# Optimization experiments

Measured on AMD Instinct MI355X. Metric: run time of the kernel, lower is better.

The kernel has to match this reference:

```python
import jax, jax.numpy as jnp
import numpy as np


def conv1x1(x, w, b):
    # x: [B,C,H,W], w: [O,C], b: [O]
    return jnp.einsum('bchw,oc->bohw', x, w) + b[None, :, None, None]


def conv3x3(x, w, b):
    # x: [B,C,H,W], w: [O,C,3,3]
    y = jax.lax.conv_general_dilated(
        x, w, window_strides=(1, 1), padding='SAME',
        dimension_numbers=('NCHW', 'OIHW', 'NCHW'))
    return y + b[None, :, None, None]


def setup_inputs() -> dict:
    key = jax.random.key(0)
    ks = jax.random.split(key, 20)

    def u(k, shape, fan_in):
        # PyTorch Conv2d default init: uniform(-1/sqrt(fan_in), 1/sqrt(fan_in))
        s = 1.0 / np.sqrt(fan_in)
        return jax.random.uniform(k, shape, jnp.float32, -s, s)

    B, H, W = 4, 64, 64
    return {
        'x':   jax.random.normal(ks[0], (B, 3, H, W), jnp.float32),
        # 1x1 stem convs (weights stored as [O,C])
        'w1':  u(ks[1], (64, 3), 3),        'b1':  u(ks[2], (64,), 3),
        'w2':  u(ks[3], (128, 64), 64),     'b2':  u(ks[4], (128,), 64),
        'w3':  u(ks[5], (256, 128), 128),   'b3':  u(ks[6], (256,), 128),
        # 3x3 conv branch (fan_in = 256*9)
        'wb1': u(ks[7], (256, 256, 3, 3), 256 * 9), 'bb1': u(ks[8], (256,), 256 * 9),
        'wb2': u(ks[9], (256, 256, 3, 3), 256 * 9), 'bb2': u(ks[10], (256,), 256 * 9),
        # q/k/v 1x1 convs
        'wq':  u(ks[11], (256, 256), 256),  'bq':  u(ks[12], (256,), 256),
        'wk':  u(ks[13], (256, 256), 256),  'bk':  u(ks[14], (256,), 256),
        'wv':  u(ks[15], (256, 256), 256),  'bv':  u(ks[16], (256,), 256),
        'alpha': jnp.float32(0.5),
        'beta':  jnp.float32(0.5),
    }


def reference(x, w1, b1, w2, b2, w3, b3, wb1, bb1, wb2, bb2,
              wq, bq, wk, bk, wv, bv, alpha, beta):
    x = jax.nn.relu(conv1x1(x, w1, b1))
    x = jax.nn.relu(conv1x1(x, w2, b2))
    x = jax.nn.relu(conv1x1(x, w3, b3))          # [B,256,H,W]
    conv_out = conv3x3(jax.nn.relu(conv3x3(x, wb1, bb1)), wb2, bb2)
    B, C, H, W = x.shape
    q = conv1x1(x, wq, bq).reshape(B, C, -1)     # [B,C,N]
    k = conv1x1(x, wk, bk).reshape(B, C, -1)     # [B,C,N]
    v = conv1x1(x, wv, bv).reshape(B, C, -1)     # [B,C,N]
    # torch: bmm(k^T, q) -> [B,N,N], softmax over last dim
    attn = jax.nn.softmax(jnp.einsum('bcn,bcm->bnm', k, q), axis=-1)
    # torch: bmm(v, attn) -> [B,C,N]
    attn_out = jnp.einsum('bcn,bnm->bcm', v, attn).reshape(B, C, H, W)
    return alpha * conv_out + beta * attn_out
```

## Files before the change

kernel.cpp:

```cpp
#include <hip/hip_runtime.h>
#include <math.h>

#define NPIX 4096
#define CC   256

typedef __attribute__((ext_vector_type(8))) short bf16x8;
typedef __attribute__((ext_vector_type(4))) float f32x4;

__device__ inline unsigned short f2bf(float f) {
    unsigned u = __builtin_bit_cast(unsigned, f);
    u += 0x7FFF + ((u >> 16) & 1);
    return (unsigned short)(u >> 16);
}
__device__ inline float bf2f(unsigned short h) {
    unsigned u = (unsigned)h << 16;
    return __builtin_bit_cast(float, u);
}
__device__ inline void gl_lds16(const void* g, void* l) {
    __builtin_amdgcn_global_load_lds(
        (const __attribute__((address_space(1))) void*)g,
        (__attribute__((address_space(3))) void*)l, 16, 0, 0);
}

__global__ __launch_bounds__(256) void prep_kernel(
    const float* __restrict__ w2, const float* __restrict__ w3,
    const float* __restrict__ wq, const float* __restrict__ wk,
    const float* __restrict__ wv, const float* __restrict__ wb1,
    const float* __restrict__ wb2, const float* __restrict__ bq,
    const float* __restrict__ bk,
    unsigned short* w2b, unsigned short* w3b, unsigned short* wqb,
    unsigned short* wkb, unsigned short* wvb,
    unsigned short* wr1, unsigned short* wr2, float* bqk) {
    int i = blockIdx.x * 256 + threadIdx.x;
    if (i < 8192)  w2b[i] = f2bf(w2[i]);
    if (i < 32768) w3b[i] = f2bf(w3[i]);
    if (i < 65536) { wqb[i] = f2bf(wq[i]); wkb[i] = f2bf(wk[i]); wvb[i] = f2bf(wv[i]); }
    if (i < 256)   { bqk[i] = bq[i]; bqk[256 + i] = bk[i]; }
    if (i < 589824) {
        int o = i / 2304; int r = i - o * 2304; int tap = r >> 8; int c = r & 255;
        wr1[i] = f2bf(wb1[(o * 256 + c) * 9 + tap]);
        wr2[i] = f2bf(wb2[(o * 256 + c) * 9 + tap]);
    }
}

__global__ __launch_bounds__(256) void stem1_kernel(
    const float* __restrict__ x, const float* __restrict__ w1,
    const float* __restrict__ b1, unsigned short* __restrict__ h1T) {
    int idx = blockIdx.x * 256 + threadIdx.x;
    int o = idx & 63;
    int p = (idx >> 6) & 4095;
    int b = idx >> 18;
    const float* xb = x + (size_t)b * 3 * NPIX + p;
    float acc = b1[o];
    acc = fmaf(w1[o * 3 + 0], xb[0],        acc);
    acc = fmaf(w1[o * 3 + 1], xb[NPIX],     acc);
    acc = fmaf(w1[o * 3 + 2], xb[2 * NPIX], acc);
    h1T[idx] = f2bf(fmaxf(acc, 0.f));
}

template<int EPI, int KK>
__global__ __launch_bounds__(256) void gemm_fullk(
    const unsigned short* __restrict__ A, long lda, long sA,
    const unsigned short* __restrict__ BT, long ldb, long sB,
    void* __restrict__ Cp, long ldc, long sC,
    const float* __restrict__ bias, float* __restrict__ aux) {
    constexpr int SPR = KK / 8;
    constexpr int RPI = 64 / SPR;
    __shared__ unsigned short As[128 * KK];
    __shared__ unsigned short Bs[128 * KK];
    const int tid  = threadIdx.x;
    const int lane = tid & 63;
    const int wave = tid >> 6;
    const int wr = (wave >> 1) * 64, wc = (wave & 1) * 64;
    const int l15 = lane & 15, lh = lane >> 4;
    const int sl  = lane & (SPR - 1);
    const int rof = lane / SPR;
    const int z = blockIdx.z;
    const unsigned short* Ab = A  + (size_t)z * sA + (size_t)blockIdx.y * 128 * lda;
    const unsigned short* Bb = BT + (size_t)z * sB + (size_t)blockIdx.x * 128 * ldb;

    f32x4 acc[4][4];
    #pragma unroll
    for (int i = 0; i < 4; ++i)
        #pragma unroll
        for (int j = 0; j < 4; ++j) { f32x4 zr = {0.f, 0.f, 0.f, 0.f}; acc[i][j] = zr; }

    #pragma unroll
    for (int i = 0; i < KK / 16; ++i) {
        int r0  = wave * 32 + i * RPI;
        int row = r0 + rof;
        int cs  = (sl ^ (row & (SPR - 1))) * 8;
        gl_lds16(Ab + (size_t)row * lda + cs, &As[r0 * KK]);
        gl_lds16(Bb + (size_t)row * ldb + cs, &Bs[r0 * KK]);
    }
    __syncthreads();

    #pragma unroll
    for (int ks = 0; ks < KK / 32; ++ks) {
        bf16x8 a[4], b[4];
        #pragma unroll
        for (int f = 0; f < 4; ++f) {
            int ra = wr + f * 16 + l15;
            a[f] = *(const bf16x8*)&As[ra * KK + ((((ks << 2) + lh) ^ (ra & (SPR - 1))) << 3)];
            int rb = wc + f * 16 + l15;
            b[f] = *(const bf16x8*)&Bs[rb * KK + ((((ks << 2) + lh) ^ (rb & (SPR - 1))) << 3)];
        }
        #pragma unroll
        for (int i = 0; i < 4; ++i)
            #pragma unroll
            for (int j = 0; j < 4; ++j)
                acc[i][j] = __builtin_amdgcn_mfma_f32_16x16x32_bf16(
                    a[i], b[j], acc[i][j], 0, 0, 0);
    }

    const int row0 = blockIdx.y * 128 + wr;
    const int col0 = blockIdx.x * 128 + wc;
    unsigned short* OUT = (unsigned short*)Cp + (size_t)z * sC;
    #pragma unroll
    for (int i = 0; i < 4; ++i)
        #pragma unroll
        for (int j = 0; j < 4; ++j) {
            int cgl = col0 + j * 16 + l15;
            float bc = (EPI == 1 || EPI == 2) ? bias[cgl] : 0.f;
            float sc = (EPI == 3) ? aux[(size_t)z * 4096 + cgl] : 1.f;
            #pragma unroll
            for (int q = 0; q < 4; ++q) {
                int r = row0 + i * 16 + lh * 4 + q;
                float v = acc[i][j][q];
                if (EPI == 3) v = (v + bias[r]) * sc;
                else v += bc;
                if (EPI == 1) v = fmaxf(v, 0.f);
                OUT[(size_t)r * ldc + cgl] = f2bf(v);
            }
        }
}

template<int EPI>
__global__ __launch_bounds__(256) void gemm128(
    const unsigned short* __restrict__ A, long lda, long sA,
    const unsigned short* __restrict__ BT, long ldb, long sB,
    int Kc, int splits, int nb,
    void* __restrict__ Cp, long ldc, long sC,
    float* __restrict__ aux, unsigned short* __restrict__ partial,
    const unsigned short* __restrict__ CV,
    const float* __restrict__ alphaP, const float* __restrict__ betaP,
    int nwgc) {
    __shared__ unsigned short As[2][128 * 64];
    __shared__ unsigned short Bs[2][128 * 64];
    const int orig = blockIdx.x;
    const int wgid = (orig & 7) * nwgc + (orig >> 3);
    int bx, by, sp, z;
    if (EPI == 0) {
        bx = wgid & 31; by = (wgid >> 5) & 31; z = wgid >> 10; sp = 0;
    } else {
        bx = wgid & 31; by = (wgid >> 5) & 1;
        sp = (wgid >> 6) % splits; z = wgid / (64 * splits);
    }

    const int tid  = threadIdx.x;
    const int lane = tid & 63;
    const int wave = tid >> 6;
    const int wr = (wave >> 1) * 64, wc = (wave & 1) * 64;
    const int l15 = lane & 15, lh = lane >> 4;
    const int sl  = lane & 7, rof = lane >> 3;
    const unsigned short* Ab = A  + (size_t)z * sA + (size_t)by * 128 * lda + (size_t)sp * Kc;
    const unsigned short* Bb = BT + (size_t)z * sB + (size_t)bx * 128 * ldb + (size_t)sp * Kc;

    f32x4 acc[4][4];
    #pragma unroll
    for (int i = 0; i < 4; ++i)
        #pragma unroll
        for (int j = 0; j < 4; ++j) { f32x4 zr = {0.f, 0.f, 0.f, 0.f}; acc[i][j] = zr; }

    auto STAGE = [&](int buf, int k0) {
        #pragma unroll
        for (int s = 0; s < 4; ++s) {
            int rb  = wave * 8 + s * 32;
            int row = rb + rof;
            int cs  = (sl ^ (row & 7)) * 8;
            gl_lds16(Ab + (size_t)row * lda + k0 + cs, &As[buf][rb * 64]);
            gl_lds16(Bb + (size_t)row * ldb + k0 + cs, &Bs[buf][rb * 64]);
        }
    };

    STAGE(0, 0);
    const int T = Kc >> 6;
    for (int t = 0; t < T; ++t) {
        const int cur = t & 1;
        if (t + 1 < T) {
            STAGE(cur ^ 1, (t + 1) << 6);
            asm volatile("s_waitcnt vmcnt(8)" ::: "memory");
        } else {
            asm volatile("s_waitcnt vmcnt(0)" ::: "memory");
        }
        __builtin_amdgcn_s_barrier();
        asm volatile("" ::: "memory");
        __builtin_amdgcn_s_setprio(1);
        #pragma unroll
        for (int ks = 0; ks < 2; ++ks) {
            bf16x8 a[4], b[4];
            #pragma unroll
            for (int f = 0; f < 4; ++f) {
                int ra = wr + f * 16 + l15;
                a[f] = *(const bf16x8*)&As[cur][ra * 64 + ((((ks << 2) + lh) ^ (ra & 7)) << 3)];
                int rb = wc + f * 16 + l15;
                b[f] = *(const bf16x8*)&Bs[cur][rb * 64 + ((((ks << 2) + lh) ^ (rb & 7)) << 3)];
            }
            #pragma unroll
            for (int i = 0; i < 4; ++i)
                #pragma unroll
                for (int j = 0; j < 4; ++j)
                    acc[i][j] = __builtin_amdgcn_mfma_f32_16x16x32_bf16(
                        a[i], b[j], acc[i][j], 0, 0, 0);
        }
        __builtin_amdgcn_s_setprio(0);
        asm volatile("" ::: "memory");
        __builtin_amdgcn_s_barrier();
    }

    if (EPI == 0) {
        unsigned short* OUT = (unsigned short*)Cp + (size_t)z * sC;
        const int row0 = by * 128 + wr;
        const int col0 = bx * 128 + wc;
        float cs4[4] = {0.f, 0.f, 0.f, 0.f};
        #pragma unroll
        for (int i = 0; i < 4; ++i)
            #pragma unroll
            for (int j = 0; j < 4; ++j) {
                int cgl = col0 + j * 16 + l15;
                #pragma unroll
                for (int q = 0; q < 4; ++q) {
                    int r = row0 + i * 16 + lh * 4 + q;
                    unsigned short h = f2bf(__expf(acc[i][j][q]));
                    OUT[(size_t)r * ldc + cgl] = h;
                    cs4[j] += bf2f(h);
                }
            }
        #pragma unroll
        for (int off = 16; off <= 32; off <<= 1)
            #pragma unroll
            for (int j = 0; j < 4; ++j)
                cs4[j] += __shfl_xor(cs4[j], off);
        if (lh == 0) {
            float* part = aux + (((size_t)z * 32 + by) * 2 + (wave >> 1)) * 4096;
            #pragma unroll
            for (int j = 0; j < 4; ++j)
                part[col0 + j * 16 + l15] = cs4[j];
        }
    } else {
        const int col0 = bx * 128 + wc;
        const int row0 = by * 128 + wr;
        if (splits == 1) {
            float* OUT = (float*)Cp + (size_t)z * sC;
            const unsigned short* CVb = CV + (size_t)z * sC;
            const float al = alphaP[0], be = betaP[0];
            #pragma unroll
            for (int i = 0; i < 4; ++i)
                #pragma unroll
                for (int j = 0; j < 4; ++j) {
                    int cgl = col0 + j * 16 + l15;
                    #pragma unroll
                    for (int q = 0; q < 4; ++q) {
                        int r = row0 + i * 16 + lh * 4 + q;
                        size_t o = (size_t)r * ldc + cgl;
                        OUT[o] = al * bf2f(CVb[o]) + be * acc[i][j][q];
                    }
                }
        } else {
            unsigned short* P = partial + ((size_t)sp * nb + z) * ((size_t)256 * 4096);
            #pragma unroll
            for (int i = 0; i < 4; ++i)
                #pragma unroll
                for (int j = 0; j < 4; ++j) {
                    int cgl = col0 + j * 16 + l15;
                    #pragma unroll
                    for (int q = 0; q < 4; ++q) {
                        int r = row0 + i * 16 + lh * 4 + q;
                        P[(size_t)r * 4096 + cgl] = f2bf(acc[i][j][q]);
                    }
                }
        }
    }
}

__global__ __launch_bounds__(256) void reduce_kernel(
    const unsigned short* __restrict__ partial, const unsigned short* __restrict__ cvb,
    const float* __restrict__ alphaP, const float* __restrict__ betaP,
    float* __restrict__ outp, int splits, long chunk) {
    long idx = ((long)blockIdx.x * 256 + threadIdx.x) * 4;
    if (idx >= chunk) return;
    float s0 = 0.f, s1 = 0.f, s2 = 0.f, s3 = 0.f;
    for (int sp = 0; sp < splits; ++sp) {
        ushort4 p = *(const ushort4*)&partial[(size_t)sp * chunk + idx];
        s0 += bf2f(p.x); s1 += bf2f(p.y); s2 += bf2f(p.z); s3 += bf2f(p.w);
    }
    ushort4 c4 = *(const ushort4*)&cvb[idx];
    const float al = alphaP[0], be = betaP[0];
    float4 r;
    r.x = al * bf2f(c4.x) + be * s0;
    r.y = al * bf2f(c4.y) + be * s1;
    r.z = al * bf2f(c4.z) + be * s2;
    r.w = al * bf2f(c4.w) + be * s3;
    *(float4*)&outp[idx] = r;
}

__global__ __launch_bounds__(256) void recip_kernel(
    const float* __restrict__ part, float* __restrict__ rcp) {
    int idx = blockIdx.x * 256 + threadIdx.x;
    int z = idx >> 12, n = idx & 4095;
    const float* pb = part + (size_t)z * 64 * 4096 + n;
    float s = 0.f;
    #pragma unroll 8
    for (int t = 0; t < 64; ++t) s += pb[(size_t)t * 4096];
    rcp[idx] = 1.f / s;
}

template<int PIXOUT>
__global__ __launch_bounds__(256) void conv3_v3(
    const unsigned short* __restrict__ X, const unsigned short* __restrict__ Wr,
    const float* __restrict__ bias, void* __restrict__ Outp) {
    __shared__ unsigned short wt[9 * 64 * 40];
    __shared__ unsigned short patch[264 * 40];
    const int tid  = threadIdx.x;
    const int lane = tid & 63;
    const int wave = tid >> 6;
    const int l15 = lane & 15, lh = lane >> 4;
    const int ob = blockIdx.x & 3;
    const int b  = blockIdx.x >> 2;
    const int h0 = blockIdx.y;
    const int obase = (wave & 1) * 32;
    const int pbase = (wave >> 1) * 64;
    const unsigned short* Xb  = X + (size_t)b * (NPIX * CC);
    const unsigned short* Wro = Wr + (size_t)ob * 64 * 2304;

    constexpr int NI = PIXOUT ? 4 : 2;
    constexpr int NJ = PIXOUT ? 2 : 4;
    f32x4 acc[NI][NJ];
    #pragma unroll
    for (int i = 0; i < NI; ++i)
        #pragma unroll
        for (int j = 0; j < NJ; ++j) { f32x4 zr = {0.f, 0.f, 0.f, 0.f}; acc[i][j] = zr; }

    for (int c0 = 0; c0 < 256; c0 += 32) {
        __syncthreads();
        #pragma unroll
        for (int t = 0; t < 5; ++t) {
            int q = t * 256 + tid;
            if (q < 1056) {
                int slot = q >> 2, cg = (q & 3) * 8;
                int r = slot / 66, w = slot - r * 66;
                int hh = h0 * 2 - 1 + r, ww = w - 1;
                int4 v = make_int4(0, 0, 0, 0);
                if ((unsigned)hh < 64u && (unsigned)ww < 64u)
                    v = *(const int4*)&Xb[(size_t)(hh * 64 + ww) * 256 + c0 + cg];
                *(int4*)&patch[slot * 40 + cg] = v;
            }
        }
        #pragma unroll
        for (int t = 0; t < 9; ++t) {
            int q = t * 256 + tid;
            int o = q / 36, rem = q - o * 36;
            int tap = rem >> 2, cg = (rem & 3) * 8;
            int4 v = *(const int4*)&Wro[(size_t)o * 2304 + tap * 256 + c0 + cg];
            *(int4*)&wt[(tap * 64 + o) * 40 + cg] = v;
        }
        __syncthreads();
        #pragma unroll
        for (int tap = 0; tap < 9; ++tap) {
            const int dy = tap / 3 - 1, dx = tap % 3 - 1;
            bf16x8 wf[2], pf[4];
            #pragma unroll
            for (int f = 0; f < 2; ++f) {
                int o = obase + f * 16 + l15;
                wf[f] = *(const bf16x8*)&wt[(tap * 64 + o) * 40 + lh * 8];
            }
            #pragma unroll
            for (int f = 0; f < 4; ++f) {
                int p = pbase + f * 16 + l15;
                int slot = ((p >> 6) + dy + 1) * 66 + (p & 63) + dx + 1;
                pf[f] = *(const bf16x8*)&patch[slot * 40 + lh * 8];
            }
            if (PIXOUT) {
                #pragma unroll
                for (int i = 0; i < NI; ++i)
                    #pragma unroll
                    for (int j = 0; j < NJ; ++j)
                        acc[i][j] = __builtin_amdgcn_mfma_f32_16x16x32_bf16(
                            pf[i], wf[j], acc[i][j], 0, 0, 0);
            } else {
                #pragma unroll
                for (int i = 0; i < NI; ++i)
                    #pragma unroll
                    for (int j = 0; j < NJ; ++j)
                        acc[i][j] = __builtin_amdgcn_mfma_f32_16x16x32_bf16(
                            wf[i], pf[j], acc[i][j], 0, 0, 0);
            }
        }
    }

    const int P0 = h0 * 128;
    if (PIXOUT) {
        unsigned short* O = (unsigned short*)Outp + (size_t)b * (NPIX * CC);
        #pragma unroll
        for (int i = 0; i < 4; ++i)
            #pragma unroll
            for (int j = 0; j < 2; ++j) {
                int o = ob * 64 + obase + j * 16 + l15;
                float bb = bias[o];
                #pragma unroll
                for (int q = 0; q < 4; ++q) {
                    int p = pbase + i * 16 + lh * 4 + q;
                    float v = fmaxf(acc[i][j][q] + bb, 0.f);
                    O[(size_t)(P0 + p) * CC + o] = f2bf(v);
                }
            }
    } else {
        unsigned short* O = (unsigned short*)Outp + (size_t)b * (CC * NPIX);
        #pragma unroll
        for (int i = 0; i < 2; ++i)
            #pragma unroll
            for (int j = 0; j < 4; ++j) {
                #pragma unroll
                for (int q = 0; q < 4; ++q) {
                    int o = ob * 64 + obase + i * 16 + lh * 4 + q;
                    int p = pbase + j * 16 + l15;
                    O[(size_t)o * NPIX + P0 + p] = f2bf(acc[i][j][q] + bias[o]);
                }
            }
    }
}

extern "C" void kernel_launch(void* const* d_in, const int* in_sizes, int n_in,
                              void* d_out, int out_size, void* d_ws, size_t ws_size,
                              hipStream_t stream) {
    const float* x   = (const float*)d_in[0];
    const float* w1  = (const float*)d_in[1];  const float* b1  = (const float*)d_in[2];
    const float* w2  = (const float*)d_in[3];  const float* b2  = (const float*)d_in[4];
    const float* w3  = (const float*)d_in[5];  const float* b3  = (const float*)d_in[6];
    const float* wb1 = (const float*)d_in[7];  const float* bb1 = (const float*)d_in[8];
    const float* wb2 = (const float*)d_in[9];  const float* bb2 = (const float*)d_in[10];
    const float* wq  = (const float*)d_in[11]; const float* bq  = (const float*)d_in[12];
    const float* wk  = (const float*)d_in[13]; const float* bk  = (const float*)d_in[14];
    const float* wv  = (const float*)d_in[15]; const float* bv  = (const float*)d_in[16];
    const float* alpha = (const float*)d_in[17];
    const float* beta  = (const float*)d_in[18];

    const size_t MB = 1 << 20;
    char* wsb = (char*)d_ws;
    unsigned short* x3T = (unsigned short*)(wsb + 0 * MB);
    unsigned short* qkT = (unsigned short*)(wsb + 8 * MB);
    unsigned short* cv  = (unsigned short*)(wsb + 24 * MB);
    unsigned short* t1T = (unsigned short*)(wsb + 32 * MB);
    unsigned short* h1T = (unsigned short*)(wsb + 32 * MB);
    unsigned short* h2T = (unsigned short*)(wsb + 34 * MB);
    unsigned short* vB  = (unsigned short*)(wsb + 40 * MB);
    unsigned short* w2b = (unsigned short*)(wsb + 48 * MB);
    unsigned short* w3b = w2b + 8192;
    unsigned short* wqb = w3b + 32768;
    unsigned short* wkb = wqb + 65536;
    unsigned short* wvb = wkb + 65536;
    unsigned short* wr1 = wvb + 65536;
    unsigned short* wr2 = wr1 + 589824;
    float*          bqk  = (float*)(wsb + 51 * MB);
    float*          part = (float*)(wsb + 52 * MB);
    float*          rcp  = (float*)(wsb + 56 * MB);
    unsigned short* ST   = (unsigned short*)(wsb + 57 * MB);
    float* out = (float*)d_out;
    const long ONEM = (long)CC * NPIX;
    const long SS = 4096L * 4096;

    int nb, splits;
    if      (ws_size >= (size_t)249 * MB) { nb = 4; splits = 8;  }
    else if (ws_size >= (size_t)185 * MB) { nb = 2; splits = 16; }
    else if (ws_size >= (size_t)121 * MB) { nb = 1; splits = 16; }
    else                                  { nb = 1; splits = 1;  }
    unsigned short* pvpart = (unsigned short*)(wsb + (size_t)(57 + nb * 32) * MB);

    prep_kernel<<<2304, 256, 0, stream>>>(w2, w3, wq, wk, wv, wb1, wb2, bq, bk,
                                          w2b, w3b, wqb, wkb, wvb, wr1, wr2, bqk);
    stem1_kernel<<<4096, 256, 0, stream>>>(x, w1, b1, h1T);

    gemm_fullk<1, 64><<<dim3(1, 32, 4), 256, 0, stream>>>(
        h1T, 64, 4096L * 64, w2b, 64, 0,
        h2T, 128, 4096L * 128, b2, nullptr);
    gemm_fullk<1, 128><<<dim3(2, 32, 4), 256, 0, stream>>>(
        h2T, 128, 4096L * 128, w3b, 128, 0,
        x3T, 256, 4096L * 256, b3, nullptr);
    gemm_fullk<2, 256><<<dim3(4, 32, 4), 256, 0, stream>>>(
        x3T, 256, 4096L * 256, wqb, 256, 0,
        qkT, 512, 4096L * 512, bqk, nullptr);
    conv3_v3<1><<<dim3(16, 32), 256, 0, stream>>>(x3T, wr1, bb1, t1T);
    conv3_v3<0><<<dim3(16, 32), 256, 0, stream>>>(t1T, wr2, bb2, cv);

    for (int b0 = 0; b0 < 4; b0 += nb) {
        int nwgS = 1024 * nb;
        gemm128<0><<<nwgS, 256, 0, stream>>>(
            qkT + (size_t)b0 * 4096 * 512, 512, 4096L * 512,
            qkT + (size_t)b0 * 4096 * 512 + 256, 512, 4096L * 512,
            256, 1, nb, ST, 4096, SS,
            part, nullptr, nullptr, nullptr, nullptr, nwgS / 8);
        recip_kernel<<<nb * 16, 256, 0, stream>>>(part, rcp);
        gemm_fullk<3, 256><<<dim3(32, 2, nb), 256, 0, stream>>>(
            wvb, 256, 0,
            x3T + (size_t)b0 * 4096 * 256, 256, 4096L * 256,
            vB, 4096, 256L * 4096, bv, rcp);
        int nwgP = 64 * splits * nb;
        gemm128<4><<<nwgP, 256, 0, stream>>>(
            vB, 4096, 256L * 4096, ST, 4096, SS,
            4096 / splits, splits, nb,
            out + (size_t)b0 * ONEM, 4096, ONEM,
            nullptr, pvpart, cv + (size_t)b0 * ONEM, alpha, beta, nwgP / 8);
        if (splits > 1)
            reduce_kernel<<<nb * 1024, 256, 0, stream>>>(
                pvpart, cv + (size_t)b0 * ONEM, alpha, beta,
                out + (size_t)b0 * ONEM, splits, (long)nb * ONEM);
    }
}
```

Before: 240.3 us.

## Use 8-wave gemm128 tiles, async weight loads in conv3, and fewer PV splits

The attention GEMM kernel moves from 4 waves to 8 waves per 128x128 tile, with each wave owning a 64x32 sub-tile. This halves the accumulators per thread and lets more waves hide latency, at the cost of more LDS reads per MFMA. The 3x3 conv now stages weights with direct global-to-LDS async loads into an unpadded 32-wide layout, removing the register round-trip, though the unpadded layout may cause bank conflicts. The split-K count for the PV GEMM drops to 1-2, which cuts partial-sum traffic and the reduce pass but gives fewer workgroups.

```diff
diff --git a/kernel.cpp b/kernel.cpp
--- a/kernel.cpp
+++ b/kernel.cpp
@@ -136,7 +136,7 @@
 }
 
 template<int EPI>
-__global__ __launch_bounds__(256) void gemm128(
+__global__ __launch_bounds__(512) void gemm128(
     const unsigned short* __restrict__ A, long lda, long sA,
     const unsigned short* __restrict__ BT, long ldb, long sB,
     int Kc, int splits, int nb,
@@ -160,22 +160,23 @@
     const int tid  = threadIdx.x;
     const int lane = tid & 63;
     const int wave = tid >> 6;
-    const int wr = (wave >> 1) * 64, wc = (wave & 1) * 64;
+    const int wr = (wave >> 2) * 64;
+    const int wc = (wave & 3) * 32;
     const int l15 = lane & 15, lh = lane >> 4;
     const int sl  = lane & 7, rof = lane >> 3;
     const unsigned short* Ab = A  + (size_t)z * sA + (size_t)by * 128 * lda + (size_t)sp * Kc;
     const unsigned short* Bb = BT + (size_t)z * sB + (size_t)bx * 128 * ldb + (size_t)sp * Kc;
 
-    f32x4 acc[4][4];
+    f32x4 acc[4][2];
     #pragma unroll
     for (int i = 0; i < 4; ++i)
         #pragma unroll
-        for (int j = 0; j < 4; ++j) { f32x4 zr = {0.f, 0.f, 0.f, 0.f}; acc[i][j] = zr; }
+        for (int j = 0; j < 2; ++j) { f32x4 zr = {0.f, 0.f, 0.f, 0.f}; acc[i][j] = zr; }
 
     auto STAGE = [&](int buf, int k0) {
         #pragma unroll
-        for (int s = 0; s < 4; ++s) {
-            int rb  = wave * 8 + s * 32;
+        for (int s = 0; s < 2; ++s) {
+            int rb  = wave * 16 + s * 8;
             int row = rb + rof;
             int cs  = (sl ^ (row & 7)) * 8;
             gl_lds16(Ab + (size_t)row * lda + k0 + cs, &As[buf][rb * 64]);
@@ -189,7 +190,7 @@
         const int cur = t & 1;
         if (t + 1 < T) {
             STAGE(cur ^ 1, (t + 1) << 6);
-            asm volatile("s_waitcnt vmcnt(8)" ::: "memory");
+            asm volatile("s_waitcnt vmcnt(4)" ::: "memory");
         } else {
             asm volatile("s_waitcnt vmcnt(0)" ::: "memory");
         }
@@ -198,18 +199,21 @@
         __builtin_amdgcn_s_setprio(1);
         #pragma unroll
         for (int ks = 0; ks < 2; ++ks) {
-            bf16x8 a[4], b[4];
+            bf16x8 a[4], b[2];
             #pragma unroll
             for (int f = 0; f < 4; ++f) {
                 int ra = wr + f * 16 + l15;
                 a[f] = *(const bf16x8*)&As[cur][ra * 64 + ((((ks << 2) + lh) ^ (ra & 7)) << 3)];
+            }
+            #pragma unroll
+            for (int f = 0; f < 2; ++f) {
                 int rb = wc + f * 16 + l15;
                 b[f] = *(const bf16x8*)&Bs[cur][rb * 64 + ((((ks << 2) + lh) ^ (rb & 7)) << 3)];
             }
             #pragma unroll
             for (int i = 0; i < 4; ++i)
                 #pragma unroll
-                for (int j = 0; j < 4; ++j)
+                for (int j = 0; j < 2; ++j)
                     acc[i][j] = __builtin_amdgcn_mfma_f32_16x16x32_bf16(
                         a[i], b[j], acc[i][j], 0, 0, 0);
         }
@@ -222,30 +226,30 @@
         unsigned short* OUT = (unsigned short*)Cp + (size_t)z * sC;
         const int row0 = by * 128 + wr;
         const int col0 = bx * 128 + wc;
-        float cs4[4] = {0.f, 0.f, 0.f, 0.f};
+        float cs2[2] = {0.f, 0.f};
         #pragma unroll
         for (int i = 0; i < 4; ++i)
             #pragma unroll
-            for (int j = 0; j < 4; ++j) {
+            for (int j = 0; j < 2; ++j) {
                 int cgl = col0 + j * 16 + l15;
                 #pragma unroll
                 for (int q = 0; q < 4; ++q) {
                     int r = row0 + i * 16 + lh * 4 + q;
                     unsigned short h = f2bf(__expf(acc[i][j][q]));
                     OUT[(size_t)r * ldc + cgl] = h;
-                    cs4[j] += bf2f(h);
+                    cs2[j] += bf2f(h);
                 }
             }
         #pragma unroll
         for (int off = 16; off <= 32; off <<= 1)
             #pragma unroll
-            for (int j = 0; j < 4; ++j)
-                cs4[j] += __shfl_xor(cs4[j], off);
+            for (int j = 0; j < 2; ++j)
+                cs2[j] += __shfl_xor(cs2[j], off);
         if (lh == 0) {
-            float* part = aux + (((size_t)z * 32 + by) * 2 + (wave >> 1)) * 4096;
-            #pragma unroll
-            for (int j = 0; j < 4; ++j)
-                part[col0 + j * 16 + l15] = cs4[j];
+            float* part = aux + (((size_t)z * 32 + by) * 2 + (wave >> 2)) * 4096;
+            #pragma unroll
+            for (int j = 0; j < 2; ++j)
+                part[col0 + j * 16 + l15] = cs2[j];
         }
     } else {
         const int col0 = bx * 128 + wc;
@@ -257,7 +261,7 @@
             #pragma unroll
             for (int i = 0; i < 4; ++i)
                 #pragma unroll
-                for (int j = 0; j < 4; ++j) {
+                for (int j = 0; j < 2; ++j) {
                     int cgl = col0 + j * 16 + l15;
                     #pragma unroll
                     for (int q = 0; q < 4; ++q) {
@@ -271,7 +275,7 @@
             #pragma unroll
             for (int i = 0; i < 4; ++i)
                 #pragma unroll
-                for (int j = 0; j < 4; ++j) {
+                for (int j = 0; j < 2; ++j) {
                     int cgl = col0 + j * 16 + l15;
                     #pragma unroll
                     for (int q = 0; q < 4; ++q) {
@@ -316,10 +320,10 @@
 }
 
 template<int PIXOUT>
-__global__ __launch_bounds__(256) void conv3_v3(
+__global__ __launch_bounds__(256) void conv3_v4(
     const unsigned short* __restrict__ X, const unsigned short* __restrict__ Wr,
     const float* __restrict__ bias, void* __restrict__ Outp) {
-    __shared__ unsigned short wt[9 * 64 * 40];
+    __shared__ unsigned short wt[9 * 64 * 32];
     __shared__ unsigned short patch[264 * 40];
     const int tid  = threadIdx.x;
     const int lane = tid & 63;
@@ -332,6 +336,7 @@
     const int pbase = (wave >> 1) * 64;
     const unsigned short* Xb  = X + (size_t)b * (NPIX * CC);
     const unsigned short* Wro = Wr + (size_t)ob * 64 * 2304;
+    const size_t wgbase = (size_t)(wave * 16 + (lane >> 2)) * 2304 + (lane & 3) * 8;
 
     constexpr int NI = PIXOUT ? 4 : 2;
     constexpr int NJ = PIXOUT ? 2 : 4;
@@ -343,6 +348,9 @@
 
     for (int c0 = 0; c0 < 256; c0 += 32) {
         __syncthreads();
+        #pragma unroll
+        for (int s = 0; s < 9; ++s)
+            gl_lds16(Wro + wgbase + s * 256 + c0, &wt[(s * 64 + wave * 16) * 32]);
         #pragma unroll
         for (int t = 0; t < 5; ++t) {
             int q = t * 256 + tid;
@@ -356,14 +364,6 @@
                 *(int4*)&patch[slot * 40 + cg] = v;
             }
         }
-        #pragma unroll
-        for (int t = 0; t < 9; ++t) {
-            int q = t * 256 + tid;
-            int o = q / 36, rem = q - o * 36;
-            int tap = rem >> 2, cg = (rem & 3) * 8;
-            int4 v = *(const int4*)&Wro[(size_t)o * 2304 + tap * 256 + c0 + cg];
-            *(int4*)&wt[(tap * 64 + o) * 40 + cg] = v;
-        }
         __syncthreads();
         #pragma unroll
         for (int tap = 0; tap < 9; ++tap) {
@@ -372,7 +372,7 @@
             #pragma unroll
             for (int f = 0; f < 2; ++f) {
                 int o = obase + f * 16 + l15;
-                wf[f] = *(const bf16x8*)&wt[(tap * 64 + o) * 40 + lh * 8];
+                wf[f] = *(const bf16x8*)&wt[(tap * 64 + o) * 32 + lh * 8];
             }
             #pragma unroll
             for (int f = 0; f < 4; ++f) {
@@ -470,10 +470,12 @@
     const long SS = 4096L * 4096;
 
     int nb, splits;
-    if      (ws_size >= (size_t)249 * MB) { nb = 4; splits = 8;  }
-    else if (ws_size >= (size_t)185 * MB) { nb = 2; splits = 16; }
-    else if (ws_size >= (size_t)121 * MB) { nb = 1; splits = 16; }
-    else                                  { nb = 1; splits = 1;  }
+    if      (ws_size >= (size_t)201 * MB) { nb = 4; splits = 2; }
+    else if (ws_size >= (size_t)185 * MB) { nb = 4; splits = 1; }
+    else if (ws_size >= (size_t)129 * MB) { nb = 2; splits = 2; }
+    else if (ws_size >= (size_t)121 * MB) { nb = 2; splits = 1; }
+    else if (ws_size >= (size_t)93  * MB) { nb = 1; splits = 2; }
+    else                                  { nb = 1; splits = 1; }
     unsigned short* pvpart = (unsigned short*)(wsb + (size_t)(57 + nb * 32) * MB);
 
     prep_kernel<<<2304, 256, 0, stream>>>(w2, w3, wq, wk, wv, wb1, wb2, bq, bk,
@@ -489,12 +491,12 @@
     gemm_fullk<2, 256><<<dim3(4, 32, 4), 256, 0, stream>>>(
         x3T, 256, 4096L * 256, wqb, 256, 0,
         qkT, 512, 4096L * 512, bqk, nullptr);
-    conv3_v3<1><<<dim3(16, 32), 256, 0, stream>>>(x3T, wr1, bb1, t1T);
-    conv3_v3<0><<<dim3(16, 32), 256, 0, stream>>>(t1T, wr2, bb2, cv);
+    conv3_v4<1><<<dim3(16, 32), 256, 0, stream>>>(x3T, wr1, bb1, t1T);
+    conv3_v4<0><<<dim3(16, 32), 256, 0, stream>>>(t1T, wr2, bb2, cv);
 
     for (int b0 = 0; b0 < 4; b0 += nb) {
         int nwgS = 1024 * nb;
-        gemm128<0><<<nwgS, 256, 0, stream>>>(
+        gemm128<0><<<nwgS, 512, 0, stream>>>(
             qkT + (size_t)b0 * 4096 * 512, 512, 4096L * 512,
             qkT + (size_t)b0 * 4096 * 512 + 256, 512, 4096L * 512,
             256, 1, nb, ST, 4096, SS,
@@ -505,7 +507,7 @@
             x3T + (size_t)b0 * 4096 * 256, 256, 4096L * 256,
             vB, 4096, 256L * 4096, bv, rcp);
         int nwgP = 64 * splits * nb;
-        gemm128<4><<<nwgP, 256, 0, stream>>>(
+        gemm128<4><<<nwgP, 512, 0, stream>>>(
             vB, 4096, 256L * 4096, ST, 4096, SS,
             4096 / splits, splits, nb,
             out + (size_t)b0 * ONEM, 4096, ONEM,
```

Measured after the change: 209.0 us. 13.0% less time.
